# Performance work log

Hardware: AMD Instinct MI355X
Metric: run time of the kernel (lower is better)

Reference implementation:

```python
import jax, jax.numpy as jnp
import numpy as np

_IDENTITY = jnp.array([1, 0, 0, 0], dtype=jnp.float32)

G, T, P, B = 512, 128, 256, 512  # num_graphs, max_terms, n_params, batch


def setup_inputs() -> dict:
    key = jax.random.key(0)
    k0, k1, k2, k3, k4 = jax.random.split(key, 5)
    psi_const = jax.random.randint(k0, (G, T), 0, 2).astype(jnp.int32)
    psi_params = jax.random.randint(k1, (G, T, P), 0, 2).astype(jnp.float32)
    phi_const = jax.random.randint(k2, (G, T), 0, 2).astype(jnp.int32)
    phi_params = jax.random.randint(k3, (G, T, P), 0, 2).astype(jnp.float32)
    param_vals = jax.random.randint(k4, (B, P), 0, 2).astype(jnp.float32)
    return {
        "psi_const": psi_const,
        "psi_params": psi_params,
        "phi_const": phi_const,
        "phi_params": phi_params,
        "param_vals": param_vals,
    }


def reference(psi_const, psi_params, phi_const, phi_params, param_vals):
    # GF(2) matmul: contract bitmasks with binary parameter values, mod 2.
    # psi_params: (G,T,P), param_vals: (B,P) -> (B,G,T)
    psi = jnp.mod(psi_const[None].astype(jnp.float32)
                  + jnp.einsum("gtp,bp->bgt", psi_params, param_vals), 2.0)
    phi = jnp.mod(phi_const[None].astype(jnp.float32)
                  + jnp.einsum("gtp,bp->bgt", phi_params, param_vals), 2.0)
    # Elementwise parity product and mod-2 sum over terms -> (B,G)
    exponent = jnp.mod(psi * phi, 2.0)
    sum_exponents = jnp.mod(jnp.sum(exponent, axis=-1), 2.0)
    # Parity-to-sign: (-1)^e = 1 - 2e, embedded as exact scalar (B,G,4)
    summands_exact = (1.0 - 2.0 * sum_exponents)[..., None] * _IDENTITY
    return summands_exact
```

## Files before the change

### kernel.cpp

```cpp
#include <hip/hip_runtime.h>

typedef unsigned long long u64;

#define G 512
#define T 128
#define P 256
#define B 512

#define WS_NEEDED 16384


__device__ __forceinline__ unsigned nzbit(unsigned u) {
    return (u | (0u - u)) >> 31;
}

__device__ __forceinline__ u64 pack64(const uint4* sv) {
    uint4 f[16];
    #pragma unroll
    for (int i = 0; i < 16; ++i) f[i] = sv[i];
    __builtin_amdgcn_sched_barrier(0);
    unsigned lo = 0, hi = 0;
    #pragma unroll
    for (int i = 0; i < 8; ++i) {
        lo |= nzbit(f[i].x) << (4 * i + 0);
        lo |= nzbit(f[i].y) << (4 * i + 1);
        lo |= nzbit(f[i].z) << (4 * i + 2);
        lo |= nzbit(f[i].w) << (4 * i + 3);
    }
    #pragma unroll
    for (int i = 8; i < 16; ++i) {
        hi |= nzbit(f[i].x) << (4 * (i - 8) + 0);
        hi |= nzbit(f[i].y) << (4 * (i - 8) + 1);
        hi |= nzbit(f[i].z) << (4 * (i - 8) + 2);
        hi |= nzbit(f[i].w) << (4 * (i - 8) + 3);
    }
    return ((u64)hi << 32) | (u64)lo;
}

__global__ __launch_bounds__(256) void pack_pv_linear_kernel(
    const float* __restrict__ pv, u64* __restrict__ out)
{
    int tid = blockIdx.x * 256 + threadIdx.x;
    out[tid] = pack64((const uint4*)(pv + (size_t)tid * 64));
}

#define LSTR 9

__global__ __launch_bounds__(512, 4) void pi_fused_kernel(
    const int*   __restrict__ psi_const,
    const int*   __restrict__ phi_const,
    const float* __restrict__ psi_params,
    const float* __restrict__ phi_params,
    const u64*   __restrict__ pv,
    float4*      __restrict__ out)
{
    __shared__ u64 lds[T * LSTR];

    const int g    = blockIdx.x;
    const int tid  = threadIdx.x;
    const int lane = tid & 63;
    const int wv   = tid >> 6;

    const size_t rowbase = (size_t)g * T * P;

    #pragma unroll
    for (int rep = 0; rep < 2; ++rep) {
        int w    = rep * 512 + tid;
        int t    = w >> 3;
        int slot = w & 7;
        int mat  = slot >> 2;
        int j    = slot & 3;
        const float* s = (mat ? phi_params : psi_params)
                         + rowbase + (size_t)t * P + j * 64;
        lds[t * LSTR + slot] = pack64((const uint4*)s);
    }
    __syncthreads();

    u64 ra[8], rb[8];
    #pragma unroll
    for (int k = 0; k < 8; ++k) ra[k] = lds[lane * LSTR + k];
    #pragma unroll
    for (int k = 0; k < 8; ++k) rb[k] = lds[(lane + 64) * LSTR + k];

    unsigned pa = ((unsigned)psi_const[g * T + lane]) & 1u;
    unsigned qa = ((unsigned)phi_const[g * T + lane]) & 1u;
    unsigned pb = ((unsigned)psi_const[g * T + lane + 64]) & 1u;
    unsigned qb = ((unsigned)phi_const[g * T + lane + 64]) & 1u;

    #pragma unroll
    for (int grp = 0; grp < 2; ++grp) {
        int b0  = wv * 64 + grp * 32;
        int b0u = __builtin_amdgcn_readfirstlane(b0);
        const u64* vp = pv + (size_t)b0u * 4;

        unsigned acc = 0;
        #pragma unroll
        for (int i = 0; i < 32; ++i) {
            u64 v0 = vp[i * 4 + 0], v1 = vp[i * 4 + 1];
            u64 v2 = vp[i * 4 + 2], v3 = vp[i * 4 + 3];
            u64 m0 = (ra[0] & v0) ^ (ra[1] & v1) ^ (ra[2] & v2) ^ (ra[3] & v3);
            u64 m1 = (ra[4] & v0) ^ (ra[5] & v1) ^ (ra[6] & v2) ^ (ra[7] & v3);
            u64 m2 = (rb[0] & v0) ^ (rb[1] & v1) ^ (rb[2] & v2) ^ (rb[3] & v3);
            u64 m3 = (rb[4] & v0) ^ (rb[5] & v1) ^ (rb[6] & v2) ^ (rb[7] & v3);
            unsigned f0 = (unsigned)m0 ^ (unsigned)(m0 >> 32);
            unsigned f1 = (unsigned)m1 ^ (unsigned)(m1 >> 32);
            unsigned f2 = (unsigned)m2 ^ (unsigned)(m2 >> 32);
            unsigned f3 = (unsigned)m3 ^ (unsigned)(m3 >> 32);
            unsigned t01 = ((unsigned)__popc(f0) ^ pa) & ((unsigned)__popc(f1) ^ qa);
            unsigned t23 = ((unsigned)__popc(f2) ^ pb) & ((unsigned)__popc(f3) ^ qb);
            acc ^= ((t01 ^ t23) & 1u) << i;
        }

        unsigned red = acc;
        #pragma unroll
        for (int m = 1; m < 64; m <<= 1)
            red ^= __shfl_xor(red, m, 64);

        if (lane < 32) {
            int b = b0u + lane;
            float s = 1.0f - 2.0f * (float)((red >> lane) & 1u);
            out[(size_t)b * G + g] = make_float4(s, 0.0f, 0.0f, 0.0f);
        }
    }
}

struct __align__(16) U64x2 { u64 x, y; };

__global__ __launch_bounds__(256) void pack_pv_kernel(
    const float* __restrict__ pv, u64* __restrict__ out)
{
    int lane = threadIdx.x & 63;
    int wave = threadIdx.x >> 6;
    int row  = blockIdx.x * 4 + wave;
    const float4* src = (const float4*)(pv + (size_t)row * P);
    float4 f = src[lane];
    u64 w0 = __ballot(f.x != 0.0f);
    u64 w1 = __ballot(f.y != 0.0f);
    u64 w2 = __ballot(f.z != 0.0f);
    u64 w3 = __ballot(f.w != 0.0f);
    if (lane == 0) {
        out[row * 4 + 0] = w0;
        out[row * 4 + 1] = w1;
        out[row * 4 + 2] = w2;
        out[row * 4 + 3] = w3;
    }
}

__global__ __launch_bounds__(512) void pi_main_kernel(
    const int*   __restrict__ psi_const,
    const float* __restrict__ psi_params,
    const int*   __restrict__ phi_const,
    const float* __restrict__ phi_params,
    const u64*   __restrict__ pv,
    float4*      __restrict__ out)
{
    __shared__ __align__(16) u64 rows[T * 8];
    __shared__ unsigned code_sm[T];

    const int g    = blockIdx.x;
    const int tid  = threadIdx.x;
    const int lane = tid & 63;
    const int wave = tid >> 6;

    if (tid < T) {
        unsigned pc = ((unsigned)psi_const[g * T + tid]) & 1u;
        unsigned qc = ((unsigned)phi_const[g * T + tid]) & 1u;
        code_sm[tid] = pc | (qc << 1);
    }

    for (int i = 0; i < 32; ++i) {
        int r = wave * 32 + i;
        int t = r & (T - 1);
        const float* mat = (r < T) ? psi_params : phi_params;
        int off = (r < T) ? 0 : 4;
        const float4* src = (const float4*)(mat + ((size_t)g * T + t) * P);
        float4 f = src[lane];
        u64 w0 = __ballot(f.x != 0.0f);
        u64 w1 = __ballot(f.y != 0.0f);
        u64 w2 = __ballot(f.z != 0.0f);
        u64 w3 = __ballot(f.w != 0.0f);
        if (lane == 0) {
            U64x2* d = (U64x2*)&rows[t * 8 + off];
            U64x2 a; a.x = w0; a.y = w1;
            U64x2 c; c.x = w2; c.y = w3;
            d[0] = a;
            d[1] = c;
        }
    }
    __syncthreads();

    const int b = tid;
    const u64* v = pv + (size_t)b * 4;
    u64 v0 = v[0], v1 = v[1], v2 = v[2], v3 = v[3];

    unsigned e = 0;
    #pragma unroll 8
    for (int t = 0; t < T; ++t) {
        const U64x2* row = (const U64x2*)&rows[t * 8];
        U64x2 p0 = row[0], p1 = row[1], q0 = row[2], q1 = row[3];
        u64 ma = (p0.x & v0) ^ (p0.y & v1) ^ (p1.x & v2) ^ (p1.y & v3);
        u64 mb = (q0.x & v0) ^ (q0.y & v1) ^ (q1.x & v2) ^ (q1.y & v3);
        unsigned c = code_sm[t];
        e ^= (((unsigned)__popcll(ma) ^ c) & ((unsigned)__popcll(mb) ^ (c >> 1)));
    }
    e &= 1u;

    float s = 1.0f - 2.0f * (float)e;
    out[(size_t)b * G + g] = make_float4(s, 0.0f, 0.0f, 0.0f);
}

extern "C" void kernel_launch(void* const* d_in, const int* in_sizes, int n_in,
                              void* d_out, int out_size, void* d_ws, size_t ws_size,
                              hipStream_t stream) {
    const int*   psi_const  = (const int*)  d_in[0];
    const float* psi_params = (const float*)d_in[1];
    const int*   phi_const  = (const int*)  d_in[2];
    const float* phi_params = (const float*)d_in[3];
    const float* param_vals = (const float*)d_in[4];

    u64* pv_ws = (u64*)d_ws;

    if (ws_size >= WS_NEEDED) {
        pack_pv_linear_kernel<<<(B * P / 64) / 256, 256, 0, stream>>>(
            param_vals, pv_ws);
        pi_fused_kernel<<<G, 512, 0, stream>>>(
            psi_const, phi_const, psi_params, phi_params,
            pv_ws, (float4*)d_out);
    } else {
        pack_pv_kernel<<<B / 4, 256, 0, stream>>>(param_vals, pv_ws);
        pi_main_kernel<<<G, 512, 0, stream>>>(psi_const, psi_params,
                                              phi_const, phi_params,
                                              pv_ws, (float4*)d_out);
    }
}
```

Before: 186.6 us.

## Split each graph across two half-term blocks with atomic XOR parity merge

Each graph is now processed by two 256-thread blocks, each covering half of the terms and all batch rows. Partial parities are merged with atomicXor into a zeroed workspace, and a separate epilogue kernel writes the output in coalesced order. The aim is more blocks and lower register pressure, giving better occupancy and memory-level parallelism while loading the parameter tensors. The cost is an extra kernel launch, atomics, and workspace zeroing folded into the pack kernel.

```diff
diff --git a/kernel.cpp b/kernel.cpp
--- a/kernel.cpp
+++ b/kernel.cpp
@@ -7,7 +7,9 @@
 #define P 256
 #define B 512
 
-#define WS_NEEDED 16384
+#define PV_OFF    0
+#define PAR_OFF   16384
+#define WS_NEEDED (PAR_OFF + (size_t)G * 16 * 4)
 
 
 __device__ __forceinline__ unsigned nzbit(unsigned u) {
@@ -37,59 +39,58 @@
     return ((u64)hi << 32) | (u64)lo;
 }
 
-__global__ __launch_bounds__(256) void pack_pv_linear_kernel(
-    const float* __restrict__ pv, u64* __restrict__ out)
+__global__ __launch_bounds__(256) void pack_pv_zero_kernel(
+    const float* __restrict__ pv, u64* __restrict__ pv_ws,
+    uint4* __restrict__ par_zero)
 {
     int tid = blockIdx.x * 256 + threadIdx.x;
-    out[tid] = pack64((const uint4*)(pv + (size_t)tid * 64));
+    pv_ws[tid] = pack64((const uint4*)(pv + (size_t)tid * 64));
+    par_zero[tid] = make_uint4(0, 0, 0, 0);
 }
 
 #define LSTR 9
 
-__global__ __launch_bounds__(512, 4) void pi_fused_kernel(
+__global__ __launch_bounds__(256, 6) void pi_half_kernel(
     const int*   __restrict__ psi_const,
     const int*   __restrict__ phi_const,
     const float* __restrict__ psi_params,
     const float* __restrict__ phi_params,
     const u64*   __restrict__ pv,
-    float4*      __restrict__ out)
-{
-    __shared__ u64 lds[T * LSTR];
-
-    const int g    = blockIdx.x;
+    unsigned*    __restrict__ par_ws)
+{
+    __shared__ u64 lds[64 * LSTR];
+
+    const int g    = blockIdx.x >> 1;
+    const int half = blockIdx.x & 1;
     const int tid  = threadIdx.x;
     const int lane = tid & 63;
     const int wv   = tid >> 6;
 
-    const size_t rowbase = (size_t)g * T * P;
+    const size_t rowbase = ((size_t)g * T + half * 64) * P;
 
     #pragma unroll
     for (int rep = 0; rep < 2; ++rep) {
-        int w    = rep * 512 + tid;
+        int w    = rep * 256 + tid;
         int t    = w >> 3;
         int slot = w & 7;
-        int mat  = slot >> 2;
-        int j    = slot & 3;
-        const float* s = (mat ? phi_params : psi_params)
-                         + rowbase + (size_t)t * P + j * 64;
+        const float* s = (slot < 4 ? psi_params : phi_params)
+                         + rowbase + (size_t)t * P + (slot & 3) * 64;
         lds[t * LSTR + slot] = pack64((const uint4*)s);
     }
     __syncthreads();
 
-    u64 ra[8], rb[8];
+    u64 ra[8];
     #pragma unroll
     for (int k = 0; k < 8; ++k) ra[k] = lds[lane * LSTR + k];
-    #pragma unroll
-    for (int k = 0; k < 8; ++k) rb[k] = lds[(lane + 64) * LSTR + k];
-
-    unsigned pa = ((unsigned)psi_const[g * T + lane]) & 1u;
-    unsigned qa = ((unsigned)phi_const[g * T + lane]) & 1u;
-    unsigned pb = ((unsigned)psi_const[g * T + lane + 64]) & 1u;
-    unsigned qb = ((unsigned)phi_const[g * T + lane + 64]) & 1u;
-
-    #pragma unroll
-    for (int grp = 0; grp < 2; ++grp) {
-        int b0  = wv * 64 + grp * 32;
+
+    const int tg = g * T + half * 64 + lane;
+    unsigned pa = ((unsigned)psi_const[tg]) & 1u;
+    unsigned qa = ((unsigned)phi_const[tg]) & 1u;
+
+    unsigned a0, a1, a2, a3;
+    #pragma unroll
+    for (int q = 0; q < 4; ++q) {
+        int b0  = wv * 128 + q * 32;
         int b0u = __builtin_amdgcn_readfirstlane(b0);
         const u64* vp = pv + (size_t)b0u * 4;
 
@@ -100,28 +101,37 @@
             u64 v2 = vp[i * 4 + 2], v3 = vp[i * 4 + 3];
             u64 m0 = (ra[0] & v0) ^ (ra[1] & v1) ^ (ra[2] & v2) ^ (ra[3] & v3);
             u64 m1 = (ra[4] & v0) ^ (ra[5] & v1) ^ (ra[6] & v2) ^ (ra[7] & v3);
-            u64 m2 = (rb[0] & v0) ^ (rb[1] & v1) ^ (rb[2] & v2) ^ (rb[3] & v3);
-            u64 m3 = (rb[4] & v0) ^ (rb[5] & v1) ^ (rb[6] & v2) ^ (rb[7] & v3);
             unsigned f0 = (unsigned)m0 ^ (unsigned)(m0 >> 32);
             unsigned f1 = (unsigned)m1 ^ (unsigned)(m1 >> 32);
-            unsigned f2 = (unsigned)m2 ^ (unsigned)(m2 >> 32);
-            unsigned f3 = (unsigned)m3 ^ (unsigned)(m3 >> 32);
             unsigned t01 = ((unsigned)__popc(f0) ^ pa) & ((unsigned)__popc(f1) ^ qa);
-            unsigned t23 = ((unsigned)__popc(f2) ^ pb) & ((unsigned)__popc(f3) ^ qb);
-            acc ^= ((t01 ^ t23) & 1u) << i;
+            acc ^= (t01 & 1u) << i;
         }
-
-        unsigned red = acc;
-        #pragma unroll
-        for (int m = 1; m < 64; m <<= 1)
-            red ^= __shfl_xor(red, m, 64);
-
-        if (lane < 32) {
-            int b = b0u + lane;
-            float s = 1.0f - 2.0f * (float)((red >> lane) & 1u);
-            out[(size_t)b * G + g] = make_float4(s, 0.0f, 0.0f, 0.0f);
-        }
-    }
+        if (q == 0) a0 = acc; else if (q == 1) a1 = acc;
+        else if (q == 2) a2 = acc; else a3 = acc;
+    }
+
+    #pragma unroll
+    for (int m = 1; m < 64; m <<= 1) {
+        a0 ^= __shfl_xor(a0, m, 64);
+        a1 ^= __shfl_xor(a1, m, 64);
+        a2 ^= __shfl_xor(a2, m, 64);
+        a3 ^= __shfl_xor(a3, m, 64);
+    }
+    if (lane < 4) {
+        unsigned myv = (lane == 0) ? a0 : (lane == 1) ? a1 : (lane == 2) ? a2 : a3;
+        atomicXor(&par_ws[g * 16 + wv * 4 + lane], myv);
+    }
+}
+
+__global__ __launch_bounds__(256) void epilogue_kernel(
+    const unsigned* __restrict__ par_ws, float4* __restrict__ out)
+{
+    int id = blockIdx.x * 256 + threadIdx.x;
+    int b  = id >> 9;
+    int gg = id & 511;
+    unsigned w = par_ws[gg * 16 + (b >> 5)];
+    float s = 1.0f - 2.0f * (float)((w >> (b & 31)) & 1u);
+    out[id] = make_float4(s, 0.0f, 0.0f, 0.0f);
 }
 
 struct __align__(16) U64x2 { u64 x, y; };
@@ -218,18 +228,21 @@
     const float* phi_params = (const float*)d_in[3];
     const float* param_vals = (const float*)d_in[4];
 
-    u64* pv_ws = (u64*)d_ws;
-
     if (ws_size >= WS_NEEDED) {
-        pack_pv_linear_kernel<<<(B * P / 64) / 256, 256, 0, stream>>>(
-            param_vals, pv_ws);
-        pi_fused_kernel<<<G, 512, 0, stream>>>(
-            psi_const, phi_const, psi_params, phi_params,
-            pv_ws, (float4*)d_out);
+        u64*      pv_ws  = (u64*)((char*)d_ws + PV_OFF);
+        unsigned* par_ws = (unsigned*)((char*)d_ws + PAR_OFF);
+
+        pack_pv_zero_kernel<<<8, 256, 0, stream>>>(
+            param_vals, pv_ws, (uint4*)par_ws);
+        pi_half_kernel<<<G * 2, 256, 0, stream>>>(
+            psi_const, phi_const, psi_params, phi_params, pv_ws, par_ws);
+        epilogue_kernel<<<(B * G) / 256, 256, 0, stream>>>(
+            par_ws, (float4*)d_out);
     } else {
-        pack_pv_kernel<<<B / 4, 256, 0, stream>>>(param_vals, pv_ws);
+        u64* pv_packed = (u64*)d_ws;
+        pack_pv_kernel<<<B / 4, 256, 0, stream>>>(param_vals, pv_packed);
         pi_main_kernel<<<G, 512, 0, stream>>>(psi_const, psi_params,
                                               phi_const, phi_params,
-                                              pv_ws, (float4*)d_out);
-    }
-}
+                                              pv_packed, (float4*)d_out);
+    }
+}
```

Measured after the change: 185.1 us. No clear change (-0.8%).
